# Optimization experiments

Measured on AMD Instinct MI355X. Metric: run time of the kernel, lower is better.

The kernel has to match this reference:

```python
import jax, jax.numpy as jnp
import numpy as np

N_HEAD = 8


def _norm(x):
    # torch: (x - x.mean()) / x.std()  -- global, unbiased std (ddof=1)
    return (x - x.mean()) / x.std(ddof=1)


def _floyd_block2(x, w_qkv, scale):
    # x: [b, n, n, c]; w_qkv: [5c, c] (torch Linear weight layout)
    x = _norm(x)
    b, n, _, c = x.shape
    qkv = x @ w_qkv.T  # [b, n, n, 5c]
    q, k1, k2, v1, v2 = jnp.split(qkv, 5, axis=-1)

    def heads(t):  # 'b i j (h d) -> b h i j d'
        return t.reshape(b, n, n, N_HEAD, c // N_HEAD).transpose(0, 3, 1, 2, 4)

    q, k1, k2, v1, v2 = map(heads, (q, k1, k2, v1, v2))
    # pivotal attention: for pair (i,j) attend over pivot p with two k/v branches
    s = (jnp.einsum('bhijd,bhipd->bhijp', q, k1)
         + jnp.einsum('bhijd,bhpjd->bhijp', q, k2)) * scale  # [b,h,i,j,p]
    a = jax.nn.softmax(s, axis=-1)
    o = (jnp.einsum('bhijp,bhipd->bhijd', a, v1)
         + jnp.einsum('bhijp,bhpjd->bhijd', a, v2))
    # 'b h i j d -> b i j (h d)'
    return o.transpose(0, 2, 3, 1, 4).reshape(b, n, n, c)


def setup_inputs() -> dict:
    key = jax.random.key(0)
    k1, k2, k3, k4 = jax.random.split(key, 4)
    b, n, c, depth = 4, 96, 256, 4
    adj = jax.random.randint(k1, (b, n, n), 0, 2, dtype=jnp.int64)
    emb_w = jax.random.normal(k2, (128, c), dtype=jnp.float32)  # std 1.0 per init_weights
    qkv_w = jax.random.normal(k3, (depth, 5 * c, c), dtype=jnp.float32) * (c ** -0.5)
    head_w = jax.random.normal(k4, (c, c), dtype=jnp.float32) * 0.02
    head_b = jnp.zeros((c,), dtype=jnp.float32)
    return {'adj': adj, 'emb_w': emb_w, 'qkv_w': qkv_w,
            'head_w': head_w, 'head_b': head_b}


def reference(adj, emb_w, qkv_w, head_w, head_b):
    c = emb_w.shape[1]
    head_dim = c // N_HEAD
    scale = head_dim ** (-0.5) * 50.0  # FloydBlock2 scale
    x = emb_w[adj]  # [b, n, n, c]
    for l in range(qkv_w.shape[0]):
        x = _floyd_block2(x, qkv_w[l], scale)
    x = x.mean(axis=(1, 2))           # mean over (i, j) -> [b, c]
    x = jax.lax.stop_gradient(x)      # blocks run under torch.no_grad
    return x @ head_w.T + head_b
```

## Files before the change

kernel.cpp:

```cpp
#include <hip/hip_runtime.h>

#define B_ 4
#define N_ 96
#define C_ 256
#define NPAIR (B_*N_*N_)
#define CE (NPAIR*C_)
#define SCALE 8.838834764831844f
#define CP 132

typedef __attribute__((ext_vector_type(4))) float f32x4;
typedef __attribute__((ext_vector_type(8))) __bf16 bf16x8;
typedef __attribute__((ext_vector_type(4))) __bf16 bf16x4;
typedef __attribute__((ext_vector_type(4))) unsigned short u16x4;
typedef __attribute__((ext_vector_type(8))) unsigned short u16x8;

__device__ __forceinline__ unsigned short f2bf(float f){
  __bf16 h = (__bf16)f;
  return __builtin_bit_cast(unsigned short, h);
}
__device__ __forceinline__ float bf2f(unsigned short u){
  union { unsigned int i; float f; } v; v.i = ((unsigned int)u) << 16; return v.f;
}

__device__ __forceinline__ void gload16(const void* g, void* l){
  __builtin_amdgcn_global_load_lds((const __attribute__((address_space(1))) unsigned int*)g,
                                   (__attribute__((address_space(3))) unsigned int*)l,
                                   16, 0, 0);
}

__global__ __launch_bounds__(256) void k_init(float* __restrict__ z){
  for (int i = threadIdx.x; i < 1536; i += 256) z[i] = 0.f;
}

__global__ __launch_bounds__(256) void k_gather(const int* __restrict__ adj,
                                                const float* __restrict__ emb,
                                                unsigned short* __restrict__ xb,
                                                float2* __restrict__ part){
  int tid = threadIdx.x;
  int lp = tid >> 4, lane16 = tid & 15;
  int pair = blockIdx.x*16 + lp;
  int row = adj[pair];
  const f32x4* src = (const f32x4*)(emb + (size_t)row*C_);
  u16x4*       dst = (u16x4*)(xb + (size_t)pair*C_);
  float s = 0.f, q = 0.f;
  for (int v = 0; v < 4; ++v){
    f32x4 t = src[v*16 + lane16];
    u16x4 o;
    o.x = f2bf(t.x); o.y = f2bf(t.y); o.z = f2bf(t.z); o.w = f2bf(t.w);
    dst[v*16 + lane16] = o;
    s += t.x + t.y + t.z + t.w;
    q += t.x*t.x + t.y*t.y + t.z*t.z + t.w*t.w;
  }
  __shared__ float rs[256], rq[256];
  rs[tid] = s; rq[tid] = q; __syncthreads();
  for (int o = 128; o > 0; o >>= 1){
    if (tid < o){ rs[tid] += rs[tid+o]; rq[tid] += rq[tid+o]; }
    __syncthreads();
  }
  if (tid == 0){
    float* pp = (float*)&part[blockIdx.x & 63];
    atomicAdd(pp, rs[0]); atomicAdd(pp+1, rq[0]);
  }
}

__global__ __launch_bounds__(256) void k_wconv(const float* __restrict__ w,
                                               unsigned short* __restrict__ wb,
                                               float* __restrict__ wsum){
  int row  = blockIdx.x*4 + (threadIdx.x >> 6);
  int lane = threadIdx.x & 63;
  f32x4 v = ((const f32x4*)(w + (size_t)row*256))[lane];
  u16x4 o;
  o.x = f2bf(v.x); o.y = f2bf(v.y); o.z = f2bf(v.z); o.w = f2bf(v.w);
  ((u16x4*)(wb + (size_t)row*256))[lane] = o;
  float s = v.x + v.y + v.z + v.w;
  for (int m = 32; m > 0; m >>= 1) s += __shfl_down(s, m);
  if (lane == 0) wsum[row] = s;
}

__global__ __launch_bounds__(256) void k_gemm(const unsigned short* __restrict__ Xb,
                                              const unsigned short* __restrict__ W,
                                              const float* __restrict__ wsum_l,
                                              const float2* __restrict__ part,
                                              unsigned short* __restrict__ qkv5){
  __shared__ unsigned short smem[128*CP];
  unsigned short* As = smem;
  unsigned short* Bs = smem + 128*64;
  const int tid = threadIdx.x;
  const int w = tid >> 6, lane = tid & 63;
  const int quad = lane >> 4, l16 = lane & 15;
  const int L = blockIdx.x;
  const int xcd = L & 7, rest = L >> 3;
  const int nt = rest % 10, kt2 = rest / 10;
  const int m0 = (xcd + 8*kt2) * 128, n0 = nt * 128;
  const int mw = (w & 1) * 64, nw = (w >> 1) * 64;
  float2 pp = part[lane];
  double S = (double)pp.x, Q = (double)pp.y;
  #pragma unroll
  for (int m = 32; m > 0; m >>= 1){ S += __shfl_xor(S, m); Q += __shfl_xor(Q, m); }
  const float mean = (float)(S / (double)CE);
  const float rstd = (float)(1.0 / sqrt((Q - S*S/(double)CE) / (double)(CE - 1)));
  f32x4 acc[4][4] = {};

  for (int kt = 0; kt < 256; kt += 64){
    const int rbase = w * 32;
    const int rowoff = lane >> 3;
    const int kg = (lane & 7) ^ rowoff;
    for (int i8 = 0; i8 < 4; ++i8){
      int row = rbase + i8*8 + rowoff;
      gload16(Xb + (size_t)(m0+row)*256 + kt + kg*8, &As[(rbase + i8*8)*64]);
      gload16(W  + (size_t)(n0+row)*256 + kt + kg*8, &Bs[(rbase + i8*8)*64]);
    }
    __syncthreads();
    for (int ks = 0; ks < 2; ++ks){
      bf16x8 af[4], bf[4];
      for (int t4 = 0; t4 < 4; ++t4){
        int rm = mw + t4*16 + l16;
        af[t4] = *(const bf16x8*)((const char*)As + rm*128 + ((((ks<<2)|quad) ^ (rm&7))*16));
        int rn = nw + t4*16 + l16;
        bf[t4] = *(const bf16x8*)((const char*)Bs + rn*128 + ((((ks<<2)|quad) ^ (rn&7))*16));
      }
      for (int mi = 0; mi < 4; ++mi)
        for (int ni = 0; ni < 4; ++ni)
          acc[mi][ni] = __builtin_amdgcn_mfma_f32_16x16x32_bf16(af[mi], bf[ni], acc[mi][ni], 0, 0, 0);
    }
    __syncthreads();
  }

  float ws[4];
  #pragma unroll
  for (int ni = 0; ni < 4; ++ni) ws[ni] = wsum_l[n0 + nw + ni*16 + l16];
  for (int mi = 0; mi < 4; ++mi)
    for (int ni = 0; ni < 4; ++ni)
      for (int r = 0; r < 4; ++r){
        int row = mw + mi*16 + quad*4 + r;
        int col = nw + ni*16 + l16;
        float val = rstd*(acc[mi][ni][r] - mean*ws[ni]);
        smem[row*CP + col] = f2bf(val);
      }
  __syncthreads();

  const int t_slab = n0 >> 8;
  const int hbase  = (n0 >> 5) & 7;
  unsigned short* slab = qkv5 + (size_t)t_slab*CE;
  const int trow = tid >> 4;
  const int tcol = (tid & 15) * 8;
  const int h  = hbase + (tcol >> 5);
  const int dd = tcol & 31;
  for (int pass = 0; pass < 8; ++pass){
    int row = pass*16 + trow;
    int gm = m0 + row;
    int b = gm / 9216; int rem = gm - b*9216;
    int ii = rem / 96, jj = rem - (rem/96)*96;
    u16x8 vv = *(const u16x8*)&smem[row*CP + tcol];
    *(u16x8*)&slab[(((size_t)(b*8+h)*96 + ii)*96 + jj)*32 + dd] = vv;
  }
}

__global__ __launch_bounds__(256) void k_scores1(const unsigned short* __restrict__ qkv5,
                                                 unsigned short* __restrict__ s1){
  __shared__ unsigned short Qs[96*40], Ks[96*40];
  int wg = blockIdx.x; int bh = wg/96, ic = wg - bh*96;
  int tid = threadIdx.x;
  size_t gslab = (size_t)wg*3072;
  const unsigned short* qp = qkv5 + 0*(size_t)CE + gslab;
  const unsigned short* kp = qkv5 + 1*(size_t)CE + gslab;
  for (int g = tid; g < 384; g += 256){
    int j = g >> 2, d8 = (g & 3)*8;
    *(u16x8*)&Qs[j*40 + d8] = *(const u16x8*)&qp[j*32 + d8];
    *(u16x8*)&Ks[j*40 + d8] = *(const u16x8*)&kp[j*32 + d8];
  }
  __syncthreads();
  int w = tid >> 6, lane = tid & 63, quad = lane >> 4, l16 = lane & 15;
  unsigned short* s1o = s1 + (size_t)bh*96*9216;
  #pragma unroll
  for (int r = 0; r < 9; ++r){
    int tile = w*9 + r; int jt = tile/6, pt = tile - jt*6;
    bf16x8 a = *(const bf16x8*)((const char*)Qs + (jt*16 + l16)*80 + quad*16);
    bf16x8 b = *(const bf16x8*)((const char*)Ks + (pt*16 + l16)*80 + quad*16);
    f32x4 cc = {0.f,0.f,0.f,0.f};
    cc = __builtin_amdgcn_mfma_f32_16x16x32_bf16(a, b, cc, 0, 0, 0);
    int col = pt*16 + l16;
    #pragma unroll
    for (int rr = 0; rr < 4; ++rr){
      int row = jt*16 + quad*4 + rr;
      _Float16 hv = (_Float16)(cc[rr] * SCALE);
      s1o[(size_t)row*9216 + ic*96 + col] = __builtin_bit_cast(unsigned short, hv);
    }
  }
}

__global__ __launch_bounds__(256) void k_attn2(const unsigned short* __restrict__ qkv5,
                                               const unsigned short* __restrict__ s1,
                                               unsigned short* __restrict__ a_out,
                                               unsigned short* __restrict__ xb,
                                               float* __restrict__ poolAcc,
                                               int last){
  __shared__ unsigned short Sh[96*100];
  __shared__ unsigned short VdM[32*100];
  __shared__ float Mx[192], Sx[192];
  float* poolL = Mx;
  const int L = blockIdx.x;
  const int virt = (L & 7)*384 + (L >> 3);
  int bh = virt/96, jj = virt - bh*96;
  int b = bh >> 3, h = bh & 7;
  int tid = threadIdx.x;
  int w = tid >> 6, lane = tid & 63, quad = lane >> 4, l16 = lane & 15;
  const unsigned short* qn  = qkv5 + 0*(size_t)CE;
  const unsigned short* k2n = qkv5 + 2*(size_t)CE;
  const unsigned short* v2n = qkv5 + 4*(size_t)CE;
  const unsigned short* s1g = s1 + ((size_t)bh*96 + jj)*9216;
  u16x4 s1v[9];
  #pragma unroll
  for (int r = 0; r < 9; ++r){
    int tile = w*9 + r; int it = tile/6, pt = tile - it*6;
    s1v[r] = *(const u16x4*)&s1g[(size_t)(it*16 + l16)*96 + pt*16 + quad*4];
  }
  if (tid < 192){ Mx[tid] = -1e30f; Sx[tid] = 0.f; }
  for (int g = tid; g < 384; g += 256){
    int d8 = (g & 3)*8, p = g >> 2;
    size_t base = (((size_t)bh*96 + p)*96 + jj)*32 + d8;
    *(u16x8*)&Sh[p*40 + d8]        = *(const u16x8*)&qn[base];
    *(u16x8*)&Sh[3840 + p*40 + d8] = *(const u16x8*)&k2n[base];
  }
  __syncthreads();
  const bool odd = (w & 1);
  const int itA = (w*9)/6, itB = itA + 1;
  const int slot = w & 1;
  f32x4 sc[9];
  float pmA = -1e30f, pmB = -1e30f;
  #pragma unroll
  for (int r = 0; r < 9; ++r){
    int tile = w*9 + r; int it = tile/6, pt = tile - it*6;
    bf16x8 a  = *(const bf16x8*)((const char*)Sh + 7680 + (pt*16 + l16)*80 + quad*16);
    bf16x8 bb = *(const bf16x8*)((const char*)Sh + (it*16 + l16)*80 + quad*16);
    f32x4 cc = {0.f,0.f,0.f,0.f};
    cc = __builtin_amdgcn_mfma_f32_16x16x32_bf16(a, bb, cc, 0, 0, 0);
    #pragma unroll
    for (int rr = 0; rr < 4; ++rr){
      _Float16 hv = __builtin_bit_cast(_Float16, (unsigned short)s1v[r][rr]);
      sc[r][rr] = cc[rr]*SCALE + (float)hv;
    }
    float t0 = fmaxf(fmaxf(sc[r][0], sc[r][1]), fmaxf(sc[r][2], sc[r][3]));
    bool inA = odd ? (r < 3) : (r < 6);
    if (inA) pmA = fmaxf(pmA, t0); else pmB = fmaxf(pmB, t0);
  }
  pmA = fmaxf(pmA, __shfl_xor(pmA, 16)); pmA = fmaxf(pmA, __shfl_xor(pmA, 32));
  pmB = fmaxf(pmB, __shfl_xor(pmB, 16)); pmB = fmaxf(pmB, __shfl_xor(pmB, 32));
  if (quad == 0){
    Mx[(itA*16 + l16)*2 + slot] = pmA;
    Mx[(itB*16 + l16)*2 + slot] = pmB;
  }
  __syncthreads();
  for (int g = tid; g < 384; g += 256){
    int d8 = (g & 3)*8, p = g >> 2;
    u16x8 v = *(const u16x8*)&v2n[(((size_t)bh*96 + p)*96 + jj)*32 + d8];
    #pragma unroll
    for (int k = 0; k < 8; ++k) VdM[(d8+k)*100 + p] = v[k];
  }
  float2 ta = *(const float2*)&Mx[(itA*16 + l16)*2];
  float2 tb = *(const float2*)&Mx[(itB*16 + l16)*2];
  float mAv = fmaxf(ta.x, ta.y), mBv = fmaxf(tb.x, tb.y);
  float sAa = 0.f, sBa = 0.f;
  #pragma unroll
  for (int r = 0; r < 9; ++r){
    bool inA = odd ? (r < 3) : (r < 6);
    float m = inA ? mAv : mBv;
    #pragma unroll
    for (int rr = 0; rr < 4; ++rr){
      float e = __expf(sc[r][rr] - m);
      sc[r][rr] = e;
      if (inA) sAa += e; else sBa += e;
    }
  }
  sAa += __shfl_xor(sAa, 16); sAa += __shfl_xor(sAa, 32);
  sBa += __shfl_xor(sBa, 16); sBa += __shfl_xor(sBa, 32);
  if (quad == 0){
    Sx[(itA*16 + l16)*2 + slot] = sAa;
    Sx[(itB*16 + l16)*2 + slot] = sBa;
  }
  __syncthreads();
  if (last && tid < 32) poolL[tid] = 0.f;
  float2 sa = *(const float2*)&Sx[(itA*16 + l16)*2];
  float2 sb = *(const float2*)&Sx[(itB*16 + l16)*2];
  float invA = 1.f/(sa.x + sa.y), invB = 1.f/(sb.x + sb.y);
  #pragma unroll
  for (int r = 0; r < 9; ++r){
    int tile = w*9 + r; int it = tile/6, pt = tile - it*6;
    bool inA = odd ? (r < 3) : (r < 6);
    float inv = inA ? invA : invB;
    u16x4 o;
    #pragma unroll
    for (int rr = 0; rr < 4; ++rr) o[rr] = f2bf(sc[r][rr] * inv);
    *(u16x4*)&Sh[(it*16 + l16)*100 + pt*16 + quad*4] = o;
  }
  __syncthreads();
  unsigned short* ap = a_out + (size_t)bh*96*9216 + (size_t)jj*96;
  for (int g = tid; g < 2304; g += 256){
    int i = g / 24, c4 = g - i*24;
    *(u16x4*)&ap[(size_t)i*9216 + c4*4] = *(const u16x4*)&Sh[i*100 + c4*4];
  }
  #pragma unroll
  for (int r = 0; r < 3; ++r){
    int tile = w*3 + r; int it = tile >> 1, dt = tile & 1;
    f32x4 cc = {0.f,0.f,0.f,0.f};
    #pragma unroll
    for (int kp3 = 0; kp3 < 3; ++kp3){
      const char* pa = (const char*)Sh + (it*16 + l16)*200 + kp3*64 + quad*16;
      bf16x4 alo = *(const bf16x4*)pa;
      bf16x4 ahi = *(const bf16x4*)(pa + 8);
      bf16x8 a = __builtin_shufflevector(alo, ahi, 0,1,2,3,4,5,6,7);
      const char* vb = (const char*)VdM + (dt*16 + l16)*200 + kp3*64 + quad*16;
      bf16x4 lo = *(const bf16x4*)vb;
      bf16x4 hi = *(const bf16x4*)(vb + 8);
      bf16x8 bbv = __builtin_shufflevector(lo, hi, 0,1,2,3,4,5,6,7);
      cc = __builtin_amdgcn_mfma_f32_16x16x32_bf16(a, bbv, cc, 0, 0, 0);
    }
    int d = dt*16 + l16;
    if (!last){
      #pragma unroll
      for (int rr = 0; rr < 4; ++rr){
        int i = it*16 + quad*4 + rr;
        xb[(((size_t)b*96 + i)*96 + jj)*256 + h*32 + d] = f2bf(cc[rr]);
      }
    } else {
      atomicAdd(&poolL[d], cc[0] + cc[1] + cc[2] + cc[3]);
    }
  }
  if (last){
    __syncthreads();
    if (tid < 32) atomicAdd(&poolAcc[b*256 + h*32 + tid], poolL[tid]);
  }
}

__global__ __launch_bounds__(256) void k_attn1(const unsigned short* __restrict__ a_in,
                                               const unsigned short* __restrict__ qkv5,
                                               unsigned short* __restrict__ xb,
                                               float2* __restrict__ statsPart,
                                               float* __restrict__ poolAcc,
                                               int last){
  __shared__ unsigned short As[96*104], Vd[32*100];
  __shared__ float redW[8];
  __shared__ float poolL[32];
  int wg = blockIdx.x; int bh = wg/96, ii = wg - bh*96;
  int b = bh >> 3, h = bh & 7;
  int tid = threadIdx.x;
  if (tid < 32) poolL[tid] = 0.f;
  const unsigned short* vp = qkv5 + 3*(size_t)CE + ((size_t)bh*96 + ii)*3072;
  for (int g = tid; g < 384; g += 256){
    int d8 = (g & 3)*8, p = g >> 2;
    u16x8 v = *(const u16x8*)&vp[p*32 + d8];
    #pragma unroll
    for (int k = 0; k < 8; ++k) Vd[(d8+k)*100 + p] = v[k];
  }
  const unsigned short* ain = a_in + ((size_t)bh*96 + ii)*9216;
  for (int g = tid; g < 1152; g += 256){
    int j = g / 12, cc = g - j*12;
    *(u16x8*)&As[j*104 + cc*8] = *(const u16x8*)&ain[j*96 + cc*8];
  }
  __syncthreads();
  int w = tid >> 6, lane = tid & 63, quad = lane >> 4, l16 = lane & 15;
  float ls = 0.f, lq = 0.f;
  #pragma unroll
  for (int r = 0; r < 3; ++r){
    int tile = w*3 + r; int jt = tile >> 1, dt = tile & 1;
    f32x4 cc = {0.f,0.f,0.f,0.f};
    #pragma unroll
    for (int kp3 = 0; kp3 < 3; ++kp3){
      bf16x8 a = *(const bf16x8*)((const char*)As + (jt*16 + l16)*208 + kp3*64 + quad*16);
      const char* vb = (const char*)Vd + (dt*16 + l16)*200 + kp3*64 + quad*16;
      bf16x4 lo = *(const bf16x4*)vb;
      bf16x4 hi = *(const bf16x4*)(vb + 8);
      bf16x8 bb = __builtin_shufflevector(lo, hi, 0,1,2,3,4,5,6,7);
      cc = __builtin_amdgcn_mfma_f32_16x16x32_bf16(a, bb, cc, 0, 0, 0);
    }
    int d = dt*16 + l16;
    if (!last){
      #pragma unroll
      for (int rr = 0; rr < 4; ++rr){
        int j = jt*16 + quad*4 + rr;
        size_t xi = (((size_t)b*96 + ii)*96 + j)*256 + h*32 + d;
        float val = bf2f(xb[xi]) + cc[rr];
        xb[xi] = f2bf(val); ls += val; lq += val*val;
      }
    } else {
      atomicAdd(&poolL[d], cc[0] + cc[1] + cc[2] + cc[3]);
    }
  }
  if (!last){
    #pragma unroll
    for (int m = 32; m > 0; m >>= 1){ ls += __shfl_down(ls, m); lq += __shfl_down(lq, m); }
    if (lane == 0){ redW[w] = ls; redW[4+w] = lq; }
    __syncthreads();
    if (tid == 0){
      float S = redW[0]+redW[1]+redW[2]+redW[3];
      float Q = redW[4]+redW[5]+redW[6]+redW[7];
      float* pp = (float*)&statsPart[blockIdx.x & 63];
      atomicAdd(pp, S); atomicAdd(pp+1, Q);
    }
  } else {
    __syncthreads();
    if (tid < 32) atomicAdd(&poolAcc[b*256 + h*32 + tid], poolL[tid]);
  }
}

__global__ __launch_bounds__(256) void k_head(const float* __restrict__ poolAcc,
                                              const float* __restrict__ hw,
                                              const float* __restrict__ hb,
                                              float* __restrict__ out){
  int b = blockIdx.x, t = threadIdx.x;
  __shared__ float xm[256];
  xm[t] = poolAcc[b*256 + t] * (1.0f/9216.0f);
  __syncthreads();
  float o = hb[t];
  for (int cc = 0; cc < 256; ++cc) o += xm[cc] * hw[t*256 + cc];
  out[b*256 + t] = o;
}

extern "C" void kernel_launch(void* const* d_in, const int* in_sizes, int n_in,
                              void* d_out, int out_size, void* d_ws, size_t ws_size,
                              hipStream_t stream){
  (void)in_sizes; (void)n_in; (void)out_size; (void)ws_size;
  const int*   adj  = (const int*)d_in[0];
  const float* emb  = (const float*)d_in[1];
  const float* qkvw = (const float*)d_in[2];
  const float* hw   = (const float*)d_in[3];
  const float* hb   = (const float*)d_in[4];

  char* p = (char*)d_ws;
  unsigned short* xb   = (unsigned short*)p; p += (size_t)CE*2;
  unsigned short* qkv5 = (unsigned short*)p; p += (size_t)5*CE*2;
  unsigned short* s1   = (unsigned short*)p; p += (size_t)32*96*9216*2;
  unsigned short* aP   = (unsigned short*)p; p += (size_t)32*96*9216*2;
  unsigned short* wbf  = (unsigned short*)p; p += (size_t)4*1280*256*2;
  float*          wsum = (float*)p;          p += (size_t)4*1280*4;
  float2*         part = (float2*)p;         p += 4*64*sizeof(float2);
  float*          pool = (float*)p;          p += 1024*sizeof(float);

  k_init  <<<dim3(1),     dim3(256), 0, stream>>>((float*)part);
  k_gather<<<dim3(2304),  dim3(256), 0, stream>>>(adj, emb, xb, part);
  k_wconv <<<dim3(1280),  dim3(256), 0, stream>>>(qkvw, wbf, wsum);
  for (int l = 0; l < 4; ++l){
    int last = (l == 3) ? 1 : 0;
    k_gemm   <<<dim3(2880),    dim3(256), 0, stream>>>(xb, wbf + (size_t)l*1280*256,
                                                       wsum + l*1280, part + l*64, qkv5);
    k_scores1<<<dim3(3072),    dim3(256), 0, stream>>>(qkv5, s1);
    k_attn2  <<<dim3(3072),    dim3(256), 0, stream>>>(qkv5, s1, aP, xb, pool, last);
    k_attn1  <<<dim3(3072),    dim3(256), 0, stream>>>(aP, qkv5, xb,
                                                       part + (l+1 < 4 ? (l+1)*64 : 0),
                                                       pool, last);
  }
  k_head<<<dim3(4), dim3(256), 0, stream>>>(pool, hw, hb, (float*)d_out);
}
```

Measured before the change: 571.2 us.

## Widen QKV GEMM tile to 128x256 with 512-thread blocks

The QKV projection GEMM now uses 8 waves per block and a 128x256 output tile instead of 128x128, halving the block count. Each block loads its activation rows once for twice as many output columns, cutting redundant reads of the X matrix. The epilogue writes the two 128-column halves through shared memory in turn, which adds barriers. More threads and accumulators per block can lower occupancy.

```diff
diff --git a/kernel.cpp b/kernel.cpp
--- a/kernel.cpp
+++ b/kernel.cpp
@@ -77,21 +77,21 @@
   if (lane == 0) wsum[row] = s;
 }
 
-__global__ __launch_bounds__(256) void k_gemm(const unsigned short* __restrict__ Xb,
+__global__ __launch_bounds__(512) void k_gemm(const unsigned short* __restrict__ Xb,
                                               const unsigned short* __restrict__ W,
                                               const float* __restrict__ wsum_l,
                                               const float2* __restrict__ part,
                                               unsigned short* __restrict__ qkv5){
-  __shared__ unsigned short smem[128*CP];
+  __shared__ unsigned short smem[24576];
   unsigned short* As = smem;
-  unsigned short* Bs = smem + 128*64;
+  unsigned short* Bs = smem + 8192;
   const int tid = threadIdx.x;
   const int w = tid >> 6, lane = tid & 63;
   const int quad = lane >> 4, l16 = lane & 15;
   const int L = blockIdx.x;
   const int xcd = L & 7, rest = L >> 3;
-  const int nt = rest % 10, kt2 = rest / 10;
-  const int m0 = (xcd + 8*kt2) * 128, n0 = nt * 128;
+  const int nt = rest % 5, kt2 = rest / 5;
+  const int m0 = (xcd + 8*kt2) * 128, n0 = nt * 256;
   const int mw = (w & 1) * 64, nw = (w >> 1) * 64;
   float2 pp = part[lane];
   double S = (double)pp.x, Q = (double)pp.y;
@@ -101,14 +101,18 @@
   const float rstd = (float)(1.0 / sqrt((Q - S*S/(double)CE) / (double)(CE - 1)));
   f32x4 acc[4][4] = {};
 
+  const int rowoff = lane >> 3;
+  const int kg = (lane & 7) ^ rowoff;
   for (int kt = 0; kt < 256; kt += 64){
-    const int rbase = w * 32;
-    const int rowoff = lane >> 3;
-    const int kg = (lane & 7) ^ rowoff;
+    #pragma unroll
+    for (int i8 = 0; i8 < 2; ++i8){
+      int row = w*16 + i8*8 + rowoff;
+      gload16(Xb + (size_t)(m0+row)*256 + kt + kg*8, &As[(w*16 + i8*8)*64]);
+    }
+    #pragma unroll
     for (int i8 = 0; i8 < 4; ++i8){
-      int row = rbase + i8*8 + rowoff;
-      gload16(Xb + (size_t)(m0+row)*256 + kt + kg*8, &As[(rbase + i8*8)*64]);
-      gload16(W  + (size_t)(n0+row)*256 + kt + kg*8, &Bs[(rbase + i8*8)*64]);
+      int row = w*32 + i8*8 + rowoff;
+      gload16(W  + (size_t)(n0+row)*256 + kt + kg*8, &Bs[(w*32 + i8*8)*64]);
     }
     __syncthreads();
     for (int ks = 0; ks < 2; ++ks){
@@ -129,30 +133,33 @@
   float ws[4];
   #pragma unroll
   for (int ni = 0; ni < 4; ++ni) ws[ni] = wsum_l[n0 + nw + ni*16 + l16];
-  for (int mi = 0; mi < 4; ++mi)
-    for (int ni = 0; ni < 4; ++ni)
-      for (int r = 0; r < 4; ++r){
-        int row = mw + mi*16 + quad*4 + r;
-        int col = nw + ni*16 + l16;
-        float val = rstd*(acc[mi][ni][r] - mean*ws[ni]);
-        smem[row*CP + col] = f2bf(val);
-      }
-  __syncthreads();
-
-  const int t_slab = n0 >> 8;
-  const int hbase  = (n0 >> 5) & 7;
-  unsigned short* slab = qkv5 + (size_t)t_slab*CE;
+
+  unsigned short* slab = qkv5 + (size_t)nt*CE;
   const int trow = tid >> 4;
   const int tcol = (tid & 15) * 8;
-  const int h  = hbase + (tcol >> 5);
-  const int dd = tcol & 31;
-  for (int pass = 0; pass < 8; ++pass){
-    int row = pass*16 + trow;
-    int gm = m0 + row;
-    int b = gm / 9216; int rem = gm - b*9216;
-    int ii = rem / 96, jj = rem - (rem/96)*96;
-    u16x8 vv = *(const u16x8*)&smem[row*CP + tcol];
-    *(u16x8*)&slab[(((size_t)(b*8+h)*96 + ii)*96 + jj)*32 + dd] = vv;
+  for (int hx = 0; hx < 2; ++hx){
+    if ((w >> 2) == hx){
+      int nwl = nw - hx*128;
+      for (int mi = 0; mi < 4; ++mi)
+        for (int ni = 0; ni < 4; ++ni)
+          for (int r = 0; r < 4; ++r){
+            int row = mw + mi*16 + quad*4 + r;
+            int col = nwl + ni*16 + l16;
+            smem[row*CP + col] = f2bf(rstd*(acc[mi][ni][r] - mean*ws[ni]));
+          }
+    }
+    __syncthreads();
+    const int h  = hx*4 + (tcol >> 5);
+    const int dd = tcol & 31;
+    for (int pass = 0; pass < 4; ++pass){
+      int row = pass*32 + trow;
+      int gm = m0 + row;
+      int b = gm / 9216; int rem = gm - b*9216;
+      int ii = rem / 96, jj = rem - (rem/96)*96;
+      u16x8 vv = *(const u16x8*)&smem[row*CP + tcol];
+      *(u16x8*)&slab[(((size_t)(b*8+h)*96 + ii)*96 + jj)*32 + dd] = vv;
+    }
+    __syncthreads();
   }
 }
 
@@ -441,7 +448,7 @@
   k_wconv <<<dim3(1280),  dim3(256), 0, stream>>>(qkvw, wbf, wsum);
   for (int l = 0; l < 4; ++l){
     int last = (l == 3) ? 1 : 0;
-    k_gemm   <<<dim3(2880),    dim3(256), 0, stream>>>(xb, wbf + (size_t)l*1280*256,
+    k_gemm   <<<dim3(1440),    dim3(512), 0, stream>>>(xb, wbf + (size_t)l*1280*256,
                                                        wsum + l*1280, part + l*64, qkv5);
     k_scores1<<<dim3(3072),    dim3(256), 0, stream>>>(qkv5, s1);
     k_attn2  <<<dim3(3072),    dim3(256), 0, stream>>>(qkv5, s1, aP, xb, pool, last);
```

After: 588.8 us. 3.1% more time.
